# Kernel optimization log

Hardware: AMD Instinct MI355X
Metric: run time of the kernel (lower is better)

The kernel has to match this reference:

```python
import jax, jax.numpy as jnp
import numpy as np

B, N, D = 8, 16384, 768   # bags, instances per bag, feature dim
C = 8                      # num_cluster
NC = 2                     # num_classes
NOR_INDEX = 0              # self.nor_index


def setup_inputs() -> dict:
    key = jax.random.key(0)
    k1, k2, k3 = jax.random.split(key, 3)
    inst_feat = jax.random.normal(k1, (B, N, D), dtype=jnp.float32)
    labels = jax.random.randint(k2, (B, N), 0, C)  # cluster assignment per instance
    head_w = jax.random.normal(k3, (NC, D), dtype=jnp.float32) * 0.02
    head_b = jnp.zeros((NC,), dtype=jnp.float32)
    return {"inst_feat": inst_feat, "labels": labels, "head_w": head_w, "head_b": head_b}


def reference(inst_feat, labels, head_w, head_b):
    # Fused equivalent of get_cluster_feat_mask + head + softmax + argmax/scatter select.
    Bq, Nq, Dq = inst_feat.shape
    # flatten (batch, cluster) into one segment id -> single segment-mean (scatter-reduce)
    seg = (jnp.arange(Bq, dtype=labels.dtype)[:, None] * C + labels).reshape(-1)  # [B*N]
    sums = jax.ops.segment_sum(inst_feat.reshape(-1, Dq), seg, num_segments=Bq * C)  # [B*C, D]
    counts = jax.ops.segment_sum(jnp.ones((Bq * Nq,), inst_feat.dtype), seg, num_segments=Bq * C)
    means = sums / jnp.maximum(counts, 1.0)[:, None]           # AdaptiveAvgPool1d(1) per cluster
    logits = means @ head_w.T + head_b                         # self.head, [B*C, NC]
    probs = jax.nn.softmax(logits, axis=-1)
    scores = (1.0 - probs[:, NOR_INDEX]).reshape(Bq, C)        # nor_index >= 0 branch
    max_idx = jnp.argmax(scores, axis=1)                       # argmax + scatter mask == gather winner
    feats = logits.reshape(Bq, C, -1)[jnp.arange(Bq), max_idx] # selected cluster logits, [B, NC]
    return feats
```

## Files before the change

### kernel.cpp

```cpp
#include <hip/hip_runtime.h>
#include <math.h>

#define BAGS 8
#define NINST 16384
#define DIM 768
#define NCLUST 8
#define NCLASS 2

constexpr int BLOCK = 256;
constexpr int WAVES_PER_BLOCK = BLOCK / 64;
constexpr int BLOCKS_PER_BAG = 256;
constexpr int NBLOCKS = BLOCKS_PER_BAG * BAGS;
constexpr int ROWS_PER_BLOCK = NINST / BLOCKS_PER_BAG;
constexpr int ROWS_PER_WAVE = ROWS_PER_BLOCK / WAVES_PER_BLOCK;
constexpr int NCOMP = NCLUST * NCLASS + NCLUST;

__global__ __launch_bounds__(BLOCK) void reduce_kernel(
    const float* __restrict__ inst,
    const int* __restrict__ labels,
    const float* __restrict__ head_w,
    float* __restrict__ ws)
{
    const int bag  = blockIdx.y;
    const int wave = threadIdx.x >> 6;
    const int lane = threadIdx.x & 63;
    const int row0 = blockIdx.x * ROWS_PER_BLOCK + wave * ROWS_PER_WAVE;

    const float4* w0p = (const float4*)(head_w);
    const float4* w1p = (const float4*)(head_w + DIM);
    float4 w0[3], w1[3];
#pragma unroll
    for (int i = 0; i < 3; ++i) {
        w0[i] = w0p[lane + i * 64];
        w1[i] = w1p[lane + i * 64];
    }

    float acc0[NCLUST], acc1[NCLUST];
    int cnt[NCLUST];
#pragma unroll
    for (int c = 0; c < NCLUST; ++c) { acc0[c] = 0.f; acc1[c] = 0.f; cnt[c] = 0; }

    const int*    lab_base = labels + (size_t)bag * NINST;
    const float4* x_base   = (const float4*)(inst + (size_t)bag * NINST * DIM);

    for (int rr = 0; rr < ROWS_PER_WAVE; rr += 4) {
        float4 x[4][3];
        int lab[4];
#pragma unroll
        for (int r = 0; r < 4; ++r) {
            const int row = row0 + rr + r;
            lab[r] = lab_base[row];
            const float4* xp = x_base + (size_t)row * (DIM / 4);
#pragma unroll
            for (int i = 0; i < 3; ++i) x[r][i] = xp[lane + i * 64];
        }
#pragma unroll
        for (int r = 0; r < 4; ++r) {
            float d0 = 0.f, d1 = 0.f;
#pragma unroll
            for (int i = 0; i < 3; ++i) {
                d0 = fmaf(x[r][i].x, w0[i].x, d0); d0 = fmaf(x[r][i].y, w0[i].y, d0);
                d0 = fmaf(x[r][i].z, w0[i].z, d0); d0 = fmaf(x[r][i].w, w0[i].w, d0);
                d1 = fmaf(x[r][i].x, w1[i].x, d1); d1 = fmaf(x[r][i].y, w1[i].y, d1);
                d1 = fmaf(x[r][i].z, w1[i].z, d1); d1 = fmaf(x[r][i].w, w1[i].w, d1);
            }
#pragma unroll
            for (int c = 0; c < NCLUST; ++c) {
                const bool m = (lab[r] == c);
                acc0[c] += m ? d0 : 0.f;
                acc1[c] += m ? d1 : 0.f;
                cnt[c]  += m ? 1 : 0;
            }
        }
    }

    __shared__ float lds_s[WAVES_PER_BLOCK][NCLUST * NCLASS];
    __shared__ float lds_c[WAVES_PER_BLOCK][NCLUST];
#pragma unroll
    for (int c = 0; c < NCLUST; ++c) {
        float a0 = acc0[c], a1 = acc1[c];
#pragma unroll
        for (int off = 32; off >= 1; off >>= 1) {
            a0 += __shfl_down(a0, off, 64);
            a1 += __shfl_down(a1, off, 64);
        }
        if (lane == 0) {
            lds_s[wave][c * 2 + 0] = a0;
            lds_s[wave][c * 2 + 1] = a1;
            lds_c[wave][c] = (float)cnt[c];
        }
    }
    __syncthreads();

    const int bid = blockIdx.y * gridDim.x + blockIdx.x;
    const int t = threadIdx.x;
    if (t < NCLUST * NCLASS) {
        const float s = lds_s[0][t] + lds_s[1][t] + lds_s[2][t] + lds_s[3][t];
        ws[t * NBLOCKS + bid] = s;
    } else if (t < NCOMP) {
        const int c = t - NCLUST * NCLASS;
        const float s = lds_c[0][c] + lds_c[1][c] + lds_c[2][c] + lds_c[3][c];
        ws[t * NBLOCKS + bid] = s;
    }
}

__global__ __launch_bounds__(256) void finalize_kernel(
    const float* __restrict__ ws,
    const float* __restrict__ head_b,
    float* __restrict__ out)
{
    __shared__ float red[BAGS][NCOMP];
    const int t = threadIdx.x;

    if (t < BAGS * NCOMP) {
        const int bag = t / NCOMP;
        const int comp = t % NCOMP;
        const float4* p = (const float4*)(ws + (size_t)comp * NBLOCKS + bag * BLOCKS_PER_BAG);
        float4 a = make_float4(0.f, 0.f, 0.f, 0.f);
#pragma unroll 4
        for (int i = 0; i < BLOCKS_PER_BAG / 4; ++i) {
            float4 v = p[i];
            a.x += v.x; a.y += v.y; a.z += v.z; a.w += v.w;
        }
        red[bag][comp] = (a.x + a.y) + (a.z + a.w);
    }
    __syncthreads();

    if (t < BAGS * NCLUST) {
        const int bag = t >> 3;
        const int c   = t & 7;

        const float denom = fmaxf(red[bag][NCLUST * NCLASS + c], 1.f);
        const float l0 = red[bag][c * 2 + 0] / denom + head_b[0];
        const float l1 = red[bag][c * 2 + 1] / denom + head_b[1];

        const float m  = fmaxf(l0, l1);
        const float e0 = expf(l0 - m);
        const float e1 = expf(l1 - m);
        const float score = 1.f - e0 / (e0 + e1);

        float bs = score; int bc = c; float bl0 = l0, bl1 = l1;
#pragma unroll
        for (int off = 1; off < 8; off <<= 1) {
            const float os  = __shfl_xor(bs, off, 64);
            const int   oc  = __shfl_xor(bc, off, 64);
            const float ol0 = __shfl_xor(bl0, off, 64);
            const float ol1 = __shfl_xor(bl1, off, 64);
            if (os > bs || (os == bs && oc < bc)) { bs = os; bc = oc; bl0 = ol0; bl1 = ol1; }
        }
        if (c == 0) {
            out[bag * NCLASS + 0] = bl0;
            out[bag * NCLASS + 1] = bl1;
        }
    }
}

extern "C" void kernel_launch(void* const* d_in, const int* in_sizes, int n_in,
                              void* d_out, int out_size, void* d_ws, size_t ws_size,
                              hipStream_t stream) {
    const float* inst   = (const float*)d_in[0];
    const int*   labels = (const int*)d_in[1];
    const float* head_w = (const float*)d_in[2];
    const float* head_b = (const float*)d_in[3];
    float* out = (float*)d_out;

    float* ws = (float*)d_ws;

    dim3 grid(BLOCKS_PER_BAG, BAGS);
    reduce_kernel<<<grid, BLOCK, 0, stream>>>(inst, labels, head_w, ws);
    finalize_kernel<<<1, 256, 0, stream>>>(ws, head_b, out);
}
```

Baseline: 530.4 us.

## Stage instance rows through LDS with direct global-to-LDS loads

Replaces per-wave register loads of instance rows with block-wide chunks of 8 rows loaded via global_load_lds into shared memory, then each wave reads its two rows from LDS. Labels for the block are preloaded into LDS. The aim is to reduce VGPR pressure and issue coalesced loads. In exchange it adds two barriers per chunk and is single-buffered, so load latency is no longer overlapped with compute.

```diff
diff --git a/kernel.cpp b/kernel.cpp
--- a/kernel.cpp
+++ b/kernel.cpp
@@ -12,8 +12,18 @@
 constexpr int BLOCKS_PER_BAG = 256;
 constexpr int NBLOCKS = BLOCKS_PER_BAG * BAGS;
 constexpr int ROWS_PER_BLOCK = NINST / BLOCKS_PER_BAG;
-constexpr int ROWS_PER_WAVE = ROWS_PER_BLOCK / WAVES_PER_BLOCK;
+constexpr int F4_PER_ROW = DIM / 4;
+constexpr int CHUNK_ROWS = 8;
+constexpr int NCHUNK = ROWS_PER_BLOCK / CHUNK_ROWS;
+constexpr int CHUNK_F4 = CHUNK_ROWS * F4_PER_ROW;
 constexpr int NCOMP = NCLUST * NCLASS + NCLUST;
+
+__device__ __forceinline__ void load_lds16(const void* g, void* l) {
+    __builtin_amdgcn_global_load_lds(
+        (const __attribute__((address_space(1))) unsigned int*)g,
+        (__attribute__((address_space(3))) unsigned int*)l,
+        16, 0, 0);
+}
 
 __global__ __launch_bounds__(BLOCK) void reduce_kernel(
     const float* __restrict__ inst,
@@ -21,10 +31,19 @@
     const float* __restrict__ head_w,
     float* __restrict__ ws)
 {
+    __shared__ float4 buf[CHUNK_F4];
+    __shared__ int    labs[ROWS_PER_BLOCK];
+    __shared__ float  lds_s[WAVES_PER_BLOCK][NCLUST * NCLASS];
+    __shared__ float  lds_c[WAVES_PER_BLOCK][NCLUST];
+
     const int bag  = blockIdx.y;
-    const int wave = threadIdx.x >> 6;
-    const int lane = threadIdx.x & 63;
-    const int row0 = blockIdx.x * ROWS_PER_BLOCK + wave * ROWS_PER_WAVE;
+    const int tid  = threadIdx.x;
+    const int wave = tid >> 6;
+    const int lane = tid & 63;
+    const int blockRow0 = blockIdx.x * ROWS_PER_BLOCK;
+
+    if (tid < ROWS_PER_BLOCK)
+        labs[tid] = labels[(size_t)bag * NINST + blockRow0 + tid];
 
     const float4* w0p = (const float4*)(head_w);
     const float4* w1p = (const float4*)(head_w + DIM);
@@ -40,42 +59,40 @@
 #pragma unroll
     for (int c = 0; c < NCLUST; ++c) { acc0[c] = 0.f; acc1[c] = 0.f; cnt[c] = 0; }
 
-    const int*    lab_base = labels + (size_t)bag * NINST;
-    const float4* x_base   = (const float4*)(inst + (size_t)bag * NINST * DIM);
+    const float4* gbase = (const float4*)(inst + (size_t)bag * NINST * DIM)
+                        + (size_t)blockRow0 * F4_PER_ROW;
 
-    for (int rr = 0; rr < ROWS_PER_WAVE; rr += 4) {
-        float4 x[4][3];
-        int lab[4];
+    for (int k = 0; k < NCHUNK; ++k) {
+        const float4* src = gbase + (size_t)k * CHUNK_F4;
 #pragma unroll
-        for (int r = 0; r < 4; ++r) {
-            const int row = row0 + rr + r;
-            lab[r] = lab_base[row];
-            const float4* xp = x_base + (size_t)row * (DIM / 4);
+        for (int j = 0; j < CHUNK_F4 / BLOCK; ++j)
+            load_lds16(src + j * BLOCK + tid, &buf[j * BLOCK + tid]);
+        __syncthreads();
+
 #pragma unroll
-            for (int i = 0; i < 3; ++i) x[r][i] = xp[lane + i * 64];
-        }
-#pragma unroll
-        for (int r = 0; r < 4; ++r) {
+        for (int r = 0; r < 2; ++r) {
+            const int row = wave * 2 + r;
+            const int lab = labs[k * CHUNK_ROWS + row];
             float d0 = 0.f, d1 = 0.f;
 #pragma unroll
             for (int i = 0; i < 3; ++i) {
-                d0 = fmaf(x[r][i].x, w0[i].x, d0); d0 = fmaf(x[r][i].y, w0[i].y, d0);
-                d0 = fmaf(x[r][i].z, w0[i].z, d0); d0 = fmaf(x[r][i].w, w0[i].w, d0);
-                d1 = fmaf(x[r][i].x, w1[i].x, d1); d1 = fmaf(x[r][i].y, w1[i].y, d1);
-                d1 = fmaf(x[r][i].z, w1[i].z, d1); d1 = fmaf(x[r][i].w, w1[i].w, d1);
+                const float4 x = buf[row * F4_PER_ROW + i * 64 + lane];
+                d0 = fmaf(x.x, w0[i].x, d0); d0 = fmaf(x.y, w0[i].y, d0);
+                d0 = fmaf(x.z, w0[i].z, d0); d0 = fmaf(x.w, w0[i].w, d0);
+                d1 = fmaf(x.x, w1[i].x, d1); d1 = fmaf(x.y, w1[i].y, d1);
+                d1 = fmaf(x.z, w1[i].z, d1); d1 = fmaf(x.w, w1[i].w, d1);
             }
 #pragma unroll
             for (int c = 0; c < NCLUST; ++c) {
-                const bool m = (lab[r] == c);
+                const bool m = (lab == c);
                 acc0[c] += m ? d0 : 0.f;
                 acc1[c] += m ? d1 : 0.f;
                 cnt[c]  += m ? 1 : 0;
             }
         }
+        __syncthreads();
     }
 
-    __shared__ float lds_s[WAVES_PER_BLOCK][NCLUST * NCLASS];
-    __shared__ float lds_c[WAVES_PER_BLOCK][NCLUST];
 #pragma unroll
     for (int c = 0; c < NCLUST; ++c) {
         float a0 = acc0[c], a1 = acc1[c];
@@ -93,14 +110,13 @@
     __syncthreads();
 
     const int bid = blockIdx.y * gridDim.x + blockIdx.x;
-    const int t = threadIdx.x;
-    if (t < NCLUST * NCLASS) {
-        const float s = lds_s[0][t] + lds_s[1][t] + lds_s[2][t] + lds_s[3][t];
-        ws[t * NBLOCKS + bid] = s;
-    } else if (t < NCOMP) {
-        const int c = t - NCLUST * NCLASS;
+    if (tid < NCLUST * NCLASS) {
+        const float s = lds_s[0][tid] + lds_s[1][tid] + lds_s[2][tid] + lds_s[3][tid];
+        ws[tid * NBLOCKS + bid] = s;
+    } else if (tid < NCOMP) {
+        const int c = tid - NCLUST * NCLASS;
         const float s = lds_c[0][c] + lds_c[1][c] + lds_c[2][c] + lds_c[3][c];
-        ws[t * NBLOCKS + bid] = s;
+        ws[tid * NBLOCKS + bid] = s;
     }
 }
 
```

New measurement: 534.2 us. Within noise of the previous version (+0.7%).
